# Optimization experiments

Hardware: AMD Instinct MI355X
Metric: run time of the kernel (lower is better)

## Reference

```python
import jax, jax.numpy as jnp
import numpy as np

BATCH, SEQ, CHANNELS, KSIZE = 4, 4096, 2048, 4


def setup_inputs() -> dict:
    key = jax.random.key(0)
    kx, kw = jax.random.split(key)
    x = jax.random.normal(kx, (BATCH, SEQ, CHANNELS), dtype=jnp.float32)
    # flax param init: normal(stddev=0.02), shape (kernel_size, channels)
    kernel = jax.random.normal(kw, (KSIZE, CHANNELS), dtype=jnp.float32) * 0.02
    return {"x": x, "kernel": kernel}


def reference(x, kernel):
    # Causal depthwise short conv: y[:, t] = silu(sum_j kernel[j] * x[:, t - j])
    # (the scan's window * kernel[::-1] unrolls to exactly this), with zero
    # left-padding of K-1 steps standing in for cache=None -> zeros.
    B, T, C = x.shape
    K = kernel.shape[0]
    kf = kernel.astype(x.dtype)
    cache = jnp.zeros((B, K - 1, C), dtype=x.dtype)
    xp = jnp.concatenate([cache, x], axis=1)  # [B, T+K-1, C]
    # Small fixed loop over kernel taps (K=4), fully parallel over time.
    y = kf[0][None, None, :] * xp[:, K - 1 : K - 1 + T, :]
    for j in range(1, K):
        y = y + kf[j][None, None, :] * xp[:, K - 1 - j : K - 1 - j + T, :]
    y = jax.nn.silu(y)
    # next_cache after the scan = last K-1 inputs of the padded stream
    next_cache = xp[:, T:, :]  # [B, K-1, C]
    return y, next_cache
```

## Files before the change

kernel.cpp:

```cpp
#include <hip/hip_runtime.h>
#include <math.h>


#define B_   4
#define T_   4096
#define C_   2048
#define K_   4
#define C4_  (C_ / 4)
#define TG_  2
#define NT_  (T_ / TG_)

typedef float f4 __attribute__((ext_vector_type(4)));

__device__ __forceinline__ float silu_f(float v) {
    return v * __builtin_amdgcn_rcpf(1.f + __expf(-v));
}

__global__ __launch_bounds__(256, 8) void dwconv_silu_kernel(
    const f4* __restrict__ x,
    const f4* __restrict__ kern,
    f4* __restrict__ y,
    f4* __restrict__ cache)
{
    const int j  = blockIdx.x * 256 + threadIdx.x;
    const int c4 = j & (C4_ - 1);
    const int tg = (j >> 9) & (NT_ - 1);
    const int b  = j >> 20;
    const int t0 = tg * TG_;

    const f4* xp = x + (((size_t)b * T_ + t0) * C4_ + c4);

    const f4 k0 = kern[0 * C4_ + c4];
    const f4 k1 = kern[1 * C4_ + c4];
    const f4 k2 = kern[2 * C4_ + c4];
    const f4 k3 = kern[3 * C4_ + c4];

    f4 m3, m2, m1;
    if (t0 >= 3) {
        m3 = xp[-3 * C4_];
        m2 = xp[-2 * C4_];
        m1 = xp[-1 * C4_];
    } else {
        const f4 z = (f4){0.f, 0.f, 0.f, 0.f};
        m3 = z;
        m2 = (t0 >= 2) ? xp[-2 * C4_] : z;
        m1 = (t0 >= 1) ? xp[-1 * C4_] : z;
    }
    const f4 a0 = xp[0 * C4_];
    const f4 a1 = xp[1 * C4_];

#define CONV1(r, a, w1, w2, w3)                                              \
    r.x = fmaf(k0.x, a.x, fmaf(k1.x, w1.x, fmaf(k2.x, w2.x, k3.x * w3.x)));  \
    r.y = fmaf(k0.y, a.y, fmaf(k1.y, w1.y, fmaf(k2.y, w2.y, k3.y * w3.y)));  \
    r.z = fmaf(k0.z, a.z, fmaf(k1.z, w1.z, fmaf(k2.z, w2.z, k3.z * w3.z)));  \
    r.w = fmaf(k0.w, a.w, fmaf(k1.w, w1.w, fmaf(k2.w, w2.w, k3.w * w3.w)));  \
    r.x = silu_f(r.x); r.y = silu_f(r.y); r.z = silu_f(r.z); r.w = silu_f(r.w);

    f4 r0, r1;
    CONV1(r0, a0, m1, m2, m3)
    CONV1(r1, a1, a0, m1, m2)
#undef CONV1

    f4* yp = y + (((size_t)b * T_ + t0) * C4_ + c4);
    yp[0 * C4_] = r0;
    yp[1 * C4_] = r1;

    if (tg == NT_ - 1) {
        f4* cb = cache + (size_t)b * (K_ - 1) * C4_ + c4;
        cb[0 * C4_] = m1;
        cb[1 * C4_] = a0;
        cb[2 * C4_] = a1;
    }
}

extern "C" void kernel_launch(void* const* d_in, const int* in_sizes, int n_in,
                              void* d_out, int out_size, void* d_ws, size_t ws_size,
                              hipStream_t stream)
{
    const f4* x    = (const f4*)d_in[0];
    const f4* kern = (const f4*)d_in[1];
    float*    out  = (float*)d_out;

    f4* y     = (f4*)out;
    f4* cache = (f4*)(out + (size_t)B_ * T_ * C_);

    const int total_threads = B_ * NT_ * C4_;
    dim3 grid(total_threads / 256);
    dim3 block(256);
    dwconv_silu_kernel<<<grid, block, 0, stream>>>(x, kern, y, cache);
}
```

Before: 232.5 us.

## Stage 8-step time tiles in LDS via direct global-to-LDS loads

Each block now covers 8 time steps for half of the channels. The 11 input rows (including the 3-row halo) are loaded straight into shared memory with global_load_lds, then each output is computed from a sliding register window. This cuts the halo re-read overhead from 5 rows per 2 outputs to 11 per 8 and uses asynchronous LDS loads. The cost is a block-wide barrier, extra LDS traffic and lower occupancy from the larger per-block tile.

Measured after the change: 233.0 us. No clear change (+0.2%).

```diff
diff --git a/kernel.cpp b/kernel.cpp
--- a/kernel.cpp
+++ b/kernel.cpp
@@ -2,13 +2,15 @@
 #include <math.h>
 
 
-#define B_   4
-#define T_   4096
-#define C_   2048
-#define K_   4
-#define C4_  (C_ / 4)
-#define TG_  2
-#define NT_  (T_ / TG_)
+#define B_     4
+#define T_     4096
+#define C_     2048
+#define K_     4
+#define C4_    (C_ / 4)
+#define TT_    8
+#define NTG_   (T_ / TT_)
+#define HC4_   256
+#define ROWS_  (TT_ + K_ - 1)
 
 typedef float f4 __attribute__((ext_vector_type(4)));
 
@@ -16,60 +18,71 @@
     return v * __builtin_amdgcn_rcpf(1.f + __expf(-v));
 }
 
-__global__ __launch_bounds__(256, 8) void dwconv_silu_kernel(
+__global__ __launch_bounds__(256, 3) void dwconv_silu_kernel(
     const f4* __restrict__ x,
     const f4* __restrict__ kern,
     f4* __restrict__ y,
     f4* __restrict__ cache)
 {
-    const int j  = blockIdx.x * 256 + threadIdx.x;
-    const int c4 = j & (C4_ - 1);
-    const int tg = (j >> 9) & (NT_ - 1);
-    const int b  = j >> 20;
-    const int t0 = tg * TG_;
+    __shared__ f4 tile[ROWS_ * HC4_];
 
-    const f4* xp = x + (((size_t)b * T_ + t0) * C4_ + c4);
+    const int bid  = blockIdx.x;
+    const int half = bid & 1;
+    const int tgrp = (bid >> 1) & (NTG_ - 1);
+    const int b    = bid >> 10;
+    const int t0   = tgrp * TT_;
+    const int tid  = threadIdx.x;
+    const int wv   = tid >> 6;
+    const int c4   = half * HC4_ + tid;
 
     const f4 k0 = kern[0 * C4_ + c4];
     const f4 k1 = kern[1 * C4_ + c4];
     const f4 k2 = kern[2 * C4_ + c4];
     const f4 k3 = kern[3 * C4_ + c4];
 
-    f4 m3, m2, m1;
-    if (t0 >= 3) {
-        m3 = xp[-3 * C4_];
-        m2 = xp[-2 * C4_];
-        m1 = xp[-1 * C4_];
-    } else {
-        const f4 z = (f4){0.f, 0.f, 0.f, 0.f};
-        m3 = z;
-        m2 = (t0 >= 2) ? xp[-2 * C4_] : z;
-        m1 = (t0 >= 1) ? xp[-1 * C4_] : z;
+    const f4* xb = x + ((size_t)b * T_ + t0 - (K_ - 1)) * C4_ + c4;
+    int rstart = 0;
+    if (t0 == 0) {
+        const f4 z = {0.f, 0.f, 0.f, 0.f};
+        tile[0 * HC4_ + tid] = z;
+        tile[1 * HC4_ + tid] = z;
+        tile[2 * HC4_ + tid] = z;
+        rstart = K_ - 1;
     }
-    const f4 a0 = xp[0 * C4_];
-    const f4 a1 = xp[1 * C4_];
+    #pragma unroll
+    for (int r = 0; r < ROWS_; ++r) {
+        if (r >= rstart) {
+            __builtin_amdgcn_global_load_lds(
+                (const __attribute__((address_space(1))) void*)(xb + (size_t)r * C4_),
+                (__attribute__((address_space(3))) void*)&tile[r * HC4_ + wv * 64],
+                16 , 0 , 0 );
+        }
+    }
+    __syncthreads();
 
-#define CONV1(r, a, w1, w2, w3)                                              \
-    r.x = fmaf(k0.x, a.x, fmaf(k1.x, w1.x, fmaf(k2.x, w2.x, k3.x * w3.x)));  \
-    r.y = fmaf(k0.y, a.y, fmaf(k1.y, w1.y, fmaf(k2.y, w2.y, k3.y * w3.y)));  \
-    r.z = fmaf(k0.z, a.z, fmaf(k1.z, w1.z, fmaf(k2.z, w2.z, k3.z * w3.z)));  \
-    r.w = fmaf(k0.w, a.w, fmaf(k1.w, w1.w, fmaf(k2.w, w2.w, k3.w * w3.w)));  \
-    r.x = silu_f(r.x); r.y = silu_f(r.y); r.z = silu_f(r.z); r.w = silu_f(r.w);
+    f4 w3 = tile[0 * HC4_ + tid];
+    f4 w2 = tile[1 * HC4_ + tid];
+    f4 w1 = tile[2 * HC4_ + tid];
 
-    f4 r0, r1;
-    CONV1(r0, a0, m1, m2, m3)
-    CONV1(r1, a1, a0, m1, m2)
-#undef CONV1
+    f4* yp = y + ((size_t)b * T_ + t0) * C4_ + c4;
+    #pragma unroll
+    for (int i = 0; i < TT_; ++i) {
+        const f4 a = tile[(K_ - 1 + i) * HC4_ + tid];
+        f4 r;
+        r.x = fmaf(k0.x, a.x, fmaf(k1.x, w1.x, fmaf(k2.x, w2.x, k3.x * w3.x)));
+        r.y = fmaf(k0.y, a.y, fmaf(k1.y, w1.y, fmaf(k2.y, w2.y, k3.y * w3.y)));
+        r.z = fmaf(k0.z, a.z, fmaf(k1.z, w1.z, fmaf(k2.z, w2.z, k3.z * w3.z)));
+        r.w = fmaf(k0.w, a.w, fmaf(k1.w, w1.w, fmaf(k2.w, w2.w, k3.w * w3.w)));
+        r.x = silu_f(r.x); r.y = silu_f(r.y); r.z = silu_f(r.z); r.w = silu_f(r.w);
+        yp[i * C4_] = r;
+        w3 = w2; w2 = w1; w1 = a;
+    }
 
-    f4* yp = y + (((size_t)b * T_ + t0) * C4_ + c4);
-    yp[0 * C4_] = r0;
-    yp[1 * C4_] = r1;
-
-    if (tg == NT_ - 1) {
+    if (tgrp == NTG_ - 1) {
         f4* cb = cache + (size_t)b * (K_ - 1) * C4_ + c4;
-        cb[0 * C4_] = m1;
-        cb[1 * C4_] = a0;
-        cb[2 * C4_] = a1;
+        cb[0 * C4_] = tile[(TT_ + 0) * HC4_ + tid];
+        cb[1 * C4_] = tile[(TT_ + 1) * HC4_ + tid];
+        cb[2 * C4_] = tile[(TT_ + 2) * HC4_ + tid];
     }
 }
 
@@ -84,8 +97,7 @@
     f4* y     = (f4*)out;
     f4* cache = (f4*)(out + (size_t)B_ * T_ * C_);
 
-    const int total_threads = B_ * NT_ * C4_;
-    dim3 grid(total_threads / 256);
+    dim3 grid(B_ * NTG_ * 2);
     dim3 block(256);
     dwconv_silu_kernel<<<grid, block, 0, stream>>>(x, kern, y, cache);
 }
```

## Stream time chunks per block with double-buffered direct-to-LDS loads

Applied to the files above, without the earlier changes.

Each block now walks a 32-step time chunk over half the channels and keeps the sliding window in registers. This stops re-reading the three halo rows for every pair of timesteps. Input rows are fetched with global_load_lds into a double-buffered shared array, and explicit vmcnt waits let the next tile load while the current one computes. The grid shrinks to 1024 blocks, with launch bounds lowered to 2 waves per SIMD. That cuts parallelism and relies on hand-tuned waitcnt counts being correct.

Measured after the change: 234.9 us. About the same (+1.0%).

```diff
diff --git a/kernel.cpp b/kernel.cpp
--- a/kernel.cpp
+++ b/kernel.cpp
@@ -2,13 +2,16 @@
 #include <math.h>
 
 
-#define B_   4
-#define T_   4096
-#define C_   2048
-#define K_   4
-#define C4_  (C_ / 4)
-#define TG_  2
-#define NT_  (T_ / TG_)
+#define B_    4
+#define T_    4096
+#define C_    2048
+#define K_    4
+#define C4_   (C_ / 4)
+#define TT_   8
+#define HC4_  256
+#define NCH_  128
+#define CHR_  (T_ / NCH_)
+#define NIT_  (CHR_ / TT_)
 
 typedef float f4 __attribute__((ext_vector_type(4)));
 
@@ -16,60 +19,84 @@
     return v * __builtin_amdgcn_rcpf(1.f + __expf(-v));
 }
 
-__global__ __launch_bounds__(256, 8) void dwconv_silu_kernel(
+__global__ __launch_bounds__(256, 2) void dwconv_silu_kernel(
     const f4* __restrict__ x,
     const f4* __restrict__ kern,
     f4* __restrict__ y,
     f4* __restrict__ cache)
 {
-    const int j  = blockIdx.x * 256 + threadIdx.x;
-    const int c4 = j & (C4_ - 1);
-    const int tg = (j >> 9) & (NT_ - 1);
-    const int b  = j >> 20;
-    const int t0 = tg * TG_;
+    __shared__ f4 buf[2][TT_ * HC4_];
 
-    const f4* xp = x + (((size_t)b * T_ + t0) * C4_ + c4);
+    const int bid   = blockIdx.x;
+    const int chunk = bid & (NCH_ - 1);
+    const int slab  = bid >> 7;
+    const int half  = slab & 1;
+    const int b     = slab >> 1;
+    const int tid   = threadIdx.x;
+    const int wv    = tid >> 6;
+    const int c4    = half * HC4_ + tid;
+    const int t0c   = chunk * CHR_;
 
     const f4 k0 = kern[0 * C4_ + c4];
     const f4 k1 = kern[1 * C4_ + c4];
     const f4 k2 = kern[2 * C4_ + c4];
     const f4 k3 = kern[3 * C4_ + c4];
 
-    f4 m3, m2, m1;
-    if (t0 >= 3) {
-        m3 = xp[-3 * C4_];
-        m2 = xp[-2 * C4_];
-        m1 = xp[-1 * C4_];
+    f4 w1, w2, w3;
+    if (t0c == 0) {
+        w1 = w2 = w3 = (f4){0.f, 0.f, 0.f, 0.f};
     } else {
-        const f4 z = (f4){0.f, 0.f, 0.f, 0.f};
-        m3 = z;
-        m2 = (t0 >= 2) ? xp[-2 * C4_] : z;
-        m1 = (t0 >= 1) ? xp[-1 * C4_] : z;
+        const f4* xh = x + ((size_t)b * T_ + t0c) * C4_ + c4;
+        w3 = xh[-3 * C4_];
+        w2 = xh[-2 * C4_];
+        w1 = xh[-1 * C4_];
     }
-    const f4 a0 = xp[0 * C4_];
-    const f4 a1 = xp[1 * C4_];
 
-#define CONV1(r, a, w1, w2, w3)                                              \
-    r.x = fmaf(k0.x, a.x, fmaf(k1.x, w1.x, fmaf(k2.x, w2.x, k3.x * w3.x)));  \
-    r.y = fmaf(k0.y, a.y, fmaf(k1.y, w1.y, fmaf(k2.y, w2.y, k3.y * w3.y)));  \
-    r.z = fmaf(k0.z, a.z, fmaf(k1.z, w1.z, fmaf(k2.z, w2.z, k3.z * w3.z)));  \
-    r.w = fmaf(k0.w, a.w, fmaf(k1.w, w1.w, fmaf(k2.w, w2.w, k3.w * w3.w)));  \
-    r.x = silu_f(r.x); r.y = silu_f(r.y); r.z = silu_f(r.z); r.w = silu_f(r.w);
+    const f4* xb = x + ((size_t)b * T_ + t0c) * C4_ + c4;
 
-    f4 r0, r1;
-    CONV1(r0, a0, m1, m2, m3)
-    CONV1(r1, a1, a0, m1, m2)
-#undef CONV1
+#define STAGE(it_) do {                                                          \
+        const f4* xs_ = xb + (size_t)(it_) * TT_ * C4_;                          \
+        _Pragma("unroll")                                                        \
+        for (int r_ = 0; r_ < TT_; ++r_)                                         \
+            __builtin_amdgcn_global_load_lds(                                    \
+                (const __attribute__((address_space(1))) void*)(xs_ + (size_t)r_ * C4_), \
+                (__attribute__((address_space(3))) void*)&buf[(it_) & 1][r_ * HC4_ + wv * 64], \
+                16, 0, 0);                                                       \
+    } while (0)
 
-    f4* yp = y + (((size_t)b * T_ + t0) * C4_ + c4);
-    yp[0 * C4_] = r0;
-    yp[1 * C4_] = r1;
+    STAGE(0);
 
-    if (tg == NT_ - 1) {
+    #pragma unroll
+    for (int it = 0; it < NIT_; ++it) {
+        if (it + 1 < NIT_) STAGE(it + 1);
+
+        if (it == 0 || it == NIT_ - 1)
+            asm volatile("s_waitcnt vmcnt(8)" ::: "memory");
+        else
+            asm volatile("s_waitcnt vmcnt(16)" ::: "memory");
+        __builtin_amdgcn_sched_barrier(0);
+
+        f4* yp = y + ((size_t)b * T_ + t0c + it * TT_) * C4_ + c4;
+        #pragma unroll
+        for (int r = 0; r < TT_; ++r) {
+            const f4 a = buf[it & 1][r * HC4_ + tid];
+            f4 o;
+            o.x = fmaf(k0.x, a.x, fmaf(k1.x, w1.x, fmaf(k2.x, w2.x, k3.x * w3.x)));
+            o.y = fmaf(k0.y, a.y, fmaf(k1.y, w1.y, fmaf(k2.y, w2.y, k3.y * w3.y)));
+            o.z = fmaf(k0.z, a.z, fmaf(k1.z, w1.z, fmaf(k2.z, w2.z, k3.z * w3.z)));
+            o.w = fmaf(k0.w, a.w, fmaf(k1.w, w1.w, fmaf(k2.w, w2.w, k3.w * w3.w)));
+            o.x = silu_f(o.x); o.y = silu_f(o.y); o.z = silu_f(o.z); o.w = silu_f(o.w);
+            yp[r * C4_] = o;
+            w3 = w2; w2 = w1; w1 = a;
+        }
+    }
+#undef STAGE
+
+    if (chunk == NCH_ - 1) {
         f4* cb = cache + (size_t)b * (K_ - 1) * C4_ + c4;
-        cb[0 * C4_] = m1;
-        cb[1 * C4_] = a0;
-        cb[2 * C4_] = a1;
+        cb[0 * C4_] = w3;
+        cb[1 * C4_] = w2;
+        cb[2 * C4_] = w1;
     }
 }
 
@@ -84,8 +111,7 @@
     f4* y     = (f4*)out;
     f4* cache = (f4*)(out + (size_t)B_ * T_ * C_);
 
-    const int total_threads = B_ * NT_ * C4_;
-    dim3 grid(total_threads / 256);
+    dim3 grid(B_ * 2 * NCH_);
     dim3 block(256);
     dwconv_silu_kernel<<<grid, block, 0, stream>>>(x, kern, y, cache);
 }
```
